# Performance work log

Measured on AMD Instinct MI355X. Metric: run time of the kernel, lower is better.

The kernel has to match this reference:

```python
import jax, jax.numpy as jnp
import numpy as np

B, L, D = 4, 4096, 768
ORDER = 2
EMB = 33      # HyenaFilter emb_dim default
FFN = 64      # filter_order
FREQ = 10.0


def setup_inputs() -> dict:
    key = jax.random.key(0)
    ks = jax.random.split(key, 10)
    def rn(i, shape, scale):
        return jax.random.normal(ks[i], shape, dtype=jnp.float32) * scale
    return {
        "u": jax.random.normal(ks[0], (B, L, D), dtype=jnp.float32),
        "W_in": rn(1, (D, (ORDER + 1) * D), 0.02),
        "b_in": jnp.zeros(((ORDER + 1) * D,), jnp.float32),
        "conv_k": rn(2, (3, (ORDER + 1) * D), 0.3),   # depthwise kernel, 3 taps
        "conv_b": jnp.zeros(((ORDER + 1) * D,), jnp.float32),
        "W1": rn(3, (EMB, FFN), 0.1),
        "b1": jnp.zeros((FFN,), jnp.float32),
        "W2": rn(4, (FFN, ORDER * D), 0.05),
        "b2": jnp.zeros((ORDER * D,), jnp.float32),
        "f_bias": rn(5, (ORDER, D), 0.05),
        "f_decay": rn(6, (ORDER, D), 0.05),
        "W_out": rn(7, (D, D), 0.02),
        "b_out": jnp.zeros((D,), jnp.float32),
    }


def _hyena_filter(W1, b1, W2, b2, f_bias, f_decay):
    # Implicit filter: sinusoidal positional features -> MLP with sin activation
    t = jnp.linspace(0.0, 1.0, L)[:, None]                      # [L,1]
    bands = jnp.linspace(0.0, float(EMB - 1), EMB)[None, :]     # [1,EMB]
    pe = jnp.sin(t * bands * FREQ)                              # [L,EMB]
    h = jnp.sin(FREQ * (pe @ W1 + b1))                          # [L,FFN]
    h = h @ W2 + b2                                             # [L,ORDER*D]
    h = h.reshape(L, ORDER, D).transpose(1, 2, 0)               # [ORDER,D,L]
    t_window = jnp.linspace(0.0, float(L), L)[None, None, :]    # [1,1,L]
    decay = jnp.exp(-jnp.exp(f_decay)[:, :, None] * t_window)   # [ORDER,D,L]
    return h * decay + f_bias[:, :, None]


def reference(u, W_in, b_in, conv_k, conv_b, W1, b1, W2, b2,
              f_bias, f_decay, W_out, b_out):
    # input projection: [B,L,D] -> [B,L,(ORDER+1)*D]
    proj = u @ W_in + b_in
    # depthwise causal conv, kernel_size=3 (pad 2 on the left)
    xp = jnp.pad(proj, ((0, 0), (2, 0), (0, 0)))
    proj = (xp[:, 0:L, :] * conv_k[0]
            + xp[:, 1:L + 1, :] * conv_k[1]
            + xp[:, 2:L + 2, :] * conv_k[2]) + conv_b
    proj = proj.reshape(B, L, ORDER + 1, D).transpose(0, 2, 3, 1)  # [B,ORDER+1,D,L]
    x = proj[:, :ORDER]   # gates, [B,ORDER,D,L]
    v = proj[:, ORDER]    # value, [B,D,L]

    h = _hyena_filter(W1, b1, W2, b2, f_bias, f_decay)  # [ORDER,D,L]

    n_fft = 2 * L  # zero-padded linear convolution via rfft
    for n in range(ORDER):
        v_f = jnp.fft.rfft(v, n=n_fft, axis=-1)          # [B,D,L+1] complex
        h_f = jnp.fft.rfft(h[n], n=n_fft, axis=-1)       # [D,L+1] complex
        y = jnp.fft.irfft(v_f * h_f[None], n=n_fft, axis=-1)[..., :L]
        v = y * x[:, n]                                   # gated recurrence

    return v.transpose(0, 2, 1) @ W_out + b_out           # [B,L,D]
```

## Files before the change

kernel.cpp:

```cpp
#include <hip/hip_runtime.h>
#include <math.h>

#define L_SEQ 4096
#define D_DIM 768
#define C3    2304
#define TAPS  32

typedef __attribute__((ext_vector_type(8))) short bf16x8;
typedef __attribute__((ext_vector_type(4))) float f32x4;

__device__ __forceinline__ unsigned short f2bf(float x) {
  union { float f; unsigned u; } v; v.f = x;
  unsigned r = v.u + 0x7FFF + ((v.u >> 16) & 1);
  return (unsigned short)(r >> 16);
}
__device__ __forceinline__ float bf2f(unsigned short u) {
  union { unsigned u; float f; } v; v.u = ((unsigned)u) << 16; return v.f;
}
__device__ __forceinline__ void gld_lds16(const void* g, void* l) {
  __builtin_amdgcn_global_load_lds((const __attribute__((address_space(1))) void*)g,
                                   (__attribute__((address_space(3))) void*)l, 16, 0, 0);
}

__global__ __launch_bounds__(256) void filt_kernel(const float* __restrict__ W1,
                                                   const float* __restrict__ b1,
                                                   const float* __restrict__ W2,
                                                   const float* __restrict__ b2,
                                                   const float* __restrict__ f_decay,
                                                   float* __restrict__ g_tab) {
  __shared__ float phi_s[2048];
  const int tid = threadIdx.x;
  #pragma unroll
  for (int it = 0; it < 8; ++it) {
    int idx = tid + it * 256;
    int t = idx >> 6, f = idx & 63;
    float tt = (float)t / 4095.0f;
    float s = b1[f];
    #pragma unroll
    for (int e = 0; e < 33; ++e)
      s += sinf(tt * (float)e * 10.0f) * W1[e * 64 + f];
    phi_s[idx] = sinf(10.0f * s);
  }
  __syncthreads();
  int idx = blockIdx.x * 256 + tid;
  int c2 = idx >> 5, t = idx & 31;
  float acc = b2[c2];
  #pragma unroll 8
  for (int f = 0; f < 64; ++f)
    acc += phi_s[t * 64 + f] * W2[f * 1536 + c2];
  float r = expf(f_decay[c2]);
  g_tab[idx] = acc * expf(-r * (float)t * (4096.0f / 4095.0f));
}

__global__ __launch_bounds__(256) void cvt_kernel(const float* __restrict__ src,
                                                  unsigned short* __restrict__ dst) {
  int idx = (blockIdx.x * 256 + threadIdx.x) * 4;
  float4 v = *(const float4*)&src[idx];
  ushort4 o;
  o.x = f2bf(v.x); o.y = f2bf(v.y); o.z = f2bf(v.z); o.w = f2bf(v.w);
  *(ushort4*)&dst[idx] = o;
}

__global__ __launch_bounds__(256) void wtrans_kernel(const float* __restrict__ W_in,
                                                     unsigned short* __restrict__ W_inT,
                                                     const float* __restrict__ W_out,
                                                     unsigned short* __restrict__ W_outT) {
  __shared__ float t[32][33];
  const int z = blockIdx.z;
  const float* src = z ? W_out : W_in;
  unsigned short* dst = z ? W_outT : W_inT;
  const int C = z ? 768 : 2304;
  const int c0 = blockIdx.x * 32, r0 = blockIdx.y * 32;
  if (c0 >= C) return;
  const int tx = threadIdx.x & 31, ty = threadIdx.x >> 5;
  #pragma unroll
  for (int rr = 0; rr < 4; ++rr)
    t[ty + rr * 8][tx] = src[(long)(r0 + ty + rr * 8) * C + c0 + tx];
  __syncthreads();
  #pragma unroll
  for (int rr = 0; rr < 4; ++rr)
    dst[(long)(c0 + ty + rr * 8) * 768 + r0 + tx] = f2bf(t[tx][ty + rr * 8]);
}

__device__ __forceinline__ void g1_vmwait(int VM) {
  if (VM == 8)      asm volatile("s_waitcnt vmcnt(8)" ::: "memory");
  else if (VM == 4) asm volatile("s_waitcnt vmcnt(4)" ::: "memory");
  else if (VM == 0) asm volatile("s_waitcnt vmcnt(0)" ::: "memory");
}

template<bool STG, int VM>
__device__ __forceinline__ void g1_step(int kt, char* smemc, int tid,
                                        int wm128, int wn64, int fm, int csel,
                                        const unsigned short* aP, const unsigned short* bP,
                                        f32x4 (&acc)[8][4]) {
  const int s = kt & 3;
  const unsigned short* As = (const unsigned short*)(smemc + s * 32768);
  const unsigned short* Bs = (const unsigned short*)(smemc + s * 32768 + 16384);
  bf16x8 af[4], bfr[4];
  #pragma unroll
  for (int i = 0; i < 4; ++i) af[i]  = *(const bf16x8*)&As[(wm128 + i * 16 + fm) * 32 + csel];
  #pragma unroll
  for (int jj = 0; jj < 4; ++jj) bfr[jj] = *(const bf16x8*)&Bs[(wn64 + jj * 16 + fm) * 32 + csel];
  if (STG) {
    const unsigned short* ap = aP + (kt + 3) * 32;
    char* d = smemc + ((kt + 3) & 3) * 32768 + tid * 16;
    gld_lds16(ap,         d);
    gld_lds16(ap + 98304, d + 8192);
  }
  asm volatile("" ::: "memory");
  __builtin_amdgcn_s_barrier();
  __builtin_amdgcn_s_setprio(1);
  __builtin_amdgcn_sched_barrier(0);
  #pragma unroll
  for (int i = 0; i < 4; ++i)
    #pragma unroll
    for (int jj = 0; jj < 4; ++jj)
      acc[i][jj] = __builtin_amdgcn_mfma_f32_16x16x32_bf16(af[i], bfr[jj], acc[i][jj], 0, 0, 0);
  __builtin_amdgcn_sched_barrier(0);
  __builtin_amdgcn_s_setprio(0);
  asm volatile("" ::: "memory");
  __builtin_amdgcn_s_barrier();
  bf16x8 ag[4];
  #pragma unroll
  for (int i = 0; i < 4; ++i) ag[i] = *(const bf16x8*)&As[(wm128 + (i + 4) * 16 + fm) * 32 + csel];
  if (STG) {
    const unsigned short* bp = bP + (kt + 3) * 32;
    char* d = smemc + ((kt + 3) & 3) * 32768 + 16384 + tid * 16;
    gld_lds16(bp,         d);
    gld_lds16(bp + 98304, d + 8192);
  }
  asm volatile("" ::: "memory");
  __builtin_amdgcn_s_barrier();
  __builtin_amdgcn_s_setprio(1);
  __builtin_amdgcn_sched_barrier(0);
  #pragma unroll
  for (int i = 0; i < 4; ++i)
    #pragma unroll
    for (int jj = 0; jj < 4; ++jj)
      acc[i + 4][jj] = __builtin_amdgcn_mfma_f32_16x16x32_bf16(ag[i], bfr[jj], acc[i + 4][jj], 0, 0, 0);
  __builtin_amdgcn_sched_barrier(0);
  __builtin_amdgcn_s_setprio(0);
  g1_vmwait(VM);
  asm volatile("" ::: "memory");
  __builtin_amdgcn_s_barrier();
}

__global__ __launch_bounds__(512, 2) void gemm1_8ph(const unsigned short* __restrict__ A,
                                                    const unsigned short* __restrict__ Bt,
                                                    const float* __restrict__ bias,
                                                    unsigned short* __restrict__ proj) {
  extern __shared__ char smemc[];
  const int tid = threadIdx.x;
  const int w = tid >> 6, lane = tid & 63;
  const int id = blockIdx.x;
  const int x8 = id & 7, jb = id >> 3;
  const int mt = x8 * 8 + jb / 9, nt = jb % 9;
  const int m0 = mt * 256, n0 = nt * 256;
  const int wm128 = (w >> 2) * 128, wn64 = (w & 3) * 64;
  const int fm = lane & 15;
  const int csel = (((lane >> 4) ^ ((fm >> 1) & 3)) << 3);
  const int q_src = ((tid & 3) ^ ((tid >> 3) & 3)) * 8;
  const unsigned short* aP = A  + (size_t)(m0 + (tid >> 2)) * 768 + q_src;
  const unsigned short* bP = Bt + (size_t)(n0 + (tid >> 2)) * 768 + q_src;
  f32x4 acc[8][4] = {};

  #pragma unroll
  for (int kt = 0; kt < 3; ++kt) {
    char* d = smemc + kt * 32768 + tid * 16;
    const unsigned short* ap = aP + kt * 32;
    const unsigned short* bp = bP + kt * 32;
    gld_lds16(ap,         d);
    gld_lds16(ap + 98304, d + 8192);
    gld_lds16(bp,         d + 16384);
    gld_lds16(bp + 98304, d + 24576);
  }
  asm volatile("s_waitcnt vmcnt(8)" ::: "memory");
  asm volatile("" ::: "memory");
  __builtin_amdgcn_s_barrier();

  #pragma unroll 1
  for (int kt = 0; kt < 21; ++kt)
    g1_step<true, 8>(kt, smemc, tid, wm128, wn64, fm, csel, aP, bP, acc);
  g1_step<false, 4>(21, smemc, tid, wm128, wn64, fm, csel, aP, bP, acc);
  g1_step<false, 0>(22, smemc, tid, wm128, wn64, fm, csel, aP, bP, acc);
  g1_step<false, -1>(23, smemc, tid, wm128, wn64, fm, csel, aP, bP, acc);

  const int b = m0 >> 12, l0 = m0 & 4095;
  float* fbuf = (float*)smemc + w * 1088;
  const int fk = lane >> 4;
  #pragma unroll
  for (int j2 = 0; j2 < 4; ++j2) {
    #pragma unroll
    for (int ih = 0; ih < 2; ++ih) {
      __syncthreads();
      #pragma unroll
      for (int i = 0; i < 4; ++i)
        *(f32x4*)&fbuf[fm * 68 + i * 16 + fk * 4] = acc[ih * 4 + i][j2];
      __syncthreads();
      #pragma unroll
      for (int p = 0; p < 4; ++p) {
        int nl = p * 4 + fk;
        int c = n0 + wn64 + j2 * 16 + nl;
        float4 v = *(float4*)&fbuf[nl * 68 + fm * 4];
        float bb = bias[c];
        ushort4 o;
        o.x = f2bf(v.x + bb); o.y = f2bf(v.y + bb);
        o.z = f2bf(v.z + bb); o.w = f2bf(v.w + bb);
        *(ushort4*)&proj[((size_t)b * C3 + c) * L_SEQ + l0 + wm128 + ih * 64 + fm * 4] = o;
      }
    }
  }
}

#define G2_BUF 12288
__global__ __launch_bounds__(256) void gemm2_mfma(const unsigned short* __restrict__ A,
                                                  const unsigned short* __restrict__ Bt,
                                                  const float* __restrict__ bias,
                                                  float* __restrict__ out) {
  __shared__ __align__(16) char smem[24576];
  const int tid = threadIdx.x;
  const int w = tid >> 6, lane = tid & 63;
  const int lr = tid >> 2, lc = tid & 3;
  const int id = blockIdx.y * 6 + blockIdx.x;
  const int x8 = id & 7, j = id >> 3;
  const int m0 = (x8 * 32 + j / 6) * 64;
  const int n0 = (j % 6) * 128;
  const int wm = (w & 1) * 32, wn = (w >> 1) * 64;
  const int fm = lane & 15, fk = lane >> 4;
  f32x4 acc[2][4] = {};
  const unsigned short* Ag = A + (size_t)(m0 + lr) * 768 + lc * 8;
  const unsigned short* Bg = Bt + (size_t)(n0 + lr) * 768 + lc * 8;

  {
    char* dst = smem + tid * 16;
    gld_lds16(Ag,            dst);
    gld_lds16(Bg,            dst + 4096);
    gld_lds16(Bg + 64 * 768, dst + 8192);
  }
  for (int kk = 0; kk < 24; ++kk) {
    const int cur = (kk & 1) * G2_BUF;
    __syncthreads();
    if (kk < 23) {
      const int k0 = (kk + 1) * 32;
      char* dst = smem + ((kk + 1) & 1) * G2_BUF + tid * 16;
      gld_lds16(Ag + k0,            dst);
      gld_lds16(Bg + k0,            dst + 4096);
      gld_lds16(Bg + k0 + 64 * 768, dst + 8192);
    }
    const unsigned short* As = (const unsigned short*)(smem + cur);
    const unsigned short* Bs = As + 2048;
    bf16x8 af[2], bfr[4];
    #pragma unroll
    for (int i = 0; i < 2; ++i) af[i]  = *(const bf16x8*)&As[(wm + i * 16 + fm) * 32 + fk * 8];
    #pragma unroll
    for (int j2 = 0; j2 < 4; ++j2) bfr[j2] = *(const bf16x8*)&Bs[(wn + j2 * 16 + fm) * 32 + fk * 8];
    #pragma unroll
    for (int i = 0; i < 2; ++i)
      #pragma unroll
      for (int j2 = 0; j2 < 4; ++j2)
        acc[i][j2] = __builtin_amdgcn_mfma_f32_16x16x32_bf16(af[i], bfr[j2], acc[i][j2], 0, 0, 0);
  }

  float* fbuf = (float*)smem + w * 1088;
  const int nf = lane & 15, mq = lane >> 4;
  float4 bb4 = *(const float4*)&bias[n0 + wn + nf * 4];
  #pragma unroll
  for (int i = 0; i < 2; ++i) {
    __syncthreads();
    #pragma unroll
    for (int cg = 0; cg < 4; ++cg)
      #pragma unroll
      for (int r = 0; r < 4; ++r)
        fbuf[(fk * 4 + r) * 68 + cg * 16 + fm] = acc[i][cg][r];
    __syncthreads();
    #pragma unroll
    for (int pass = 0; pass < 4; ++pass) {
      int m_l = pass * 4 + mq;
      float4 v = *(float4*)&fbuf[m_l * 68 + nf * 4];
      v.x += bb4.x; v.y += bb4.y; v.z += bb4.z; v.w += bb4.w;
      *(float4*)&out[(size_t)(m0 + wm + i * 16 + m_l) * D_DIM + n0 + wn + nf * 4] = v;
    }
  }
}

__global__ __launch_bounds__(256) void row_kernel(const unsigned short* __restrict__ proj,
                                                  unsigned short* __restrict__ v2T,
                                                  const float* __restrict__ conv_k,
                                                  const float* __restrict__ conv_b,
                                                  const float* __restrict__ g_tab,
                                                  const float* __restrict__ f_bias) {
  __shared__ float buf0[4128];
  __shared__ float buf1[4128];
  __shared__ float sgs[2 * TAPS];
  __shared__ float wsum[4];
  __shared__ float bnd[3][4][2];
  const int tid = threadIdx.x;
  const int lane = tid & 63, w = tid >> 6;
  const int b = blockIdx.x / D_DIM, d = blockIdx.x % D_DIM;
  const int g = tid * 16;

  const unsigned short* rowV  = proj + ((size_t)b * C3 + 2 * D_DIM + d) * L_SEQ;
  const unsigned short* rowX0 = proj + ((size_t)b * C3 + d) * L_SEQ;
  const unsigned short* rowX1 = proj + ((size_t)b * C3 + D_DIM + d) * L_SEQ;

  float v[16], x0[16], x1[16];
  #pragma unroll
  for (int k = 0; k < 4; ++k) {
    ushort4 qv = *(const ushort4*)&rowV[g + k * 4];
    v[k * 4] = bf2f(qv.x); v[k * 4 + 1] = bf2f(qv.y); v[k * 4 + 2] = bf2f(qv.z); v[k * 4 + 3] = bf2f(qv.w);
    ushort4 q0 = *(const ushort4*)&rowX0[g + k * 4];
    x0[k * 4] = bf2f(q0.x); x0[k * 4 + 1] = bf2f(q0.y); x0[k * 4 + 2] = bf2f(q0.z); x0[k * 4 + 3] = bf2f(q0.w);
    ushort4 q1 = *(const ushort4*)&rowX1[g + k * 4];
    x1[k * 4] = bf2f(q1.x); x1[k * 4 + 1] = bf2f(q1.y); x1[k * 4 + 2] = bf2f(q1.z); x1[k * 4 + 3] = bf2f(q1.w);
  }

  if (tid < 32) {
    int ph = (tid & 15) * 258 + (tid >> 4);
    buf0[ph] = 0.f; buf1[ph] = 0.f;
  }
  if (tid < 64) sgs[tid] = g_tab[((size_t)((tid >> 5) * D_DIM + d)) * TAPS + (tid & 31)];
  if (lane == 63) {
    bnd[0][w][0] = v[14];  bnd[0][w][1] = v[15];
    bnd[1][w][0] = x0[14]; bnd[1][w][1] = x0[15];
    bnd[2][w][0] = x1[14]; bnd[2][w][1] = x1[15];
  }
  const int cv = 2 * D_DIM + d, cx0 = d, cx1 = D_DIM + d;
  const float kv0 = conv_k[cv],  kv1 = conv_k[C3 + cv],  kv2 = conv_k[2 * C3 + cv],  bv = conv_b[cv];
  const float ka0 = conv_k[cx0], ka1 = conv_k[C3 + cx0], ka2 = conv_k[2 * C3 + cx0], ba = conv_b[cx0];
  const float kb0 = conv_k[cx1], kb1 = conv_k[C3 + cx1], kb2 = conv_k[2 * C3 + cx1], bb = conv_b[cx1];
  const float fb0 = f_bias[d], fb1 = f_bias[D_DIM + d];
  __syncthreads();

  float vm1 = __shfl_up(v[15], 1),  vm2 = __shfl_up(v[14], 1);
  float am1 = __shfl_up(x0[15], 1), am2 = __shfl_up(x0[14], 1);
  float bm1 = __shfl_up(x1[15], 1), bm2 = __shfl_up(x1[14], 1);
  if (lane == 0) {
    if (w > 0) {
      vm2 = bnd[0][w-1][0]; vm1 = bnd[0][w-1][1];
      am2 = bnd[1][w-1][0]; am1 = bnd[1][w-1][1];
      bm2 = bnd[2][w-1][0]; bm1 = bnd[2][w-1][1];
    } else {
      vm1 = vm2 = am1 = am2 = bm1 = bm2 = 0.f;
    }
  }
  float r[16];
  r[0] = vm2 * kv0 + vm1 * kv1 + v[0] * kv2 + bv;
  r[1] = vm1 * kv0 + v[0] * kv1 + v[1] * kv2 + bv;
  #pragma unroll
  for (int i = 2; i < 16; ++i) r[i] = v[i-2] * kv0 + v[i-1] * kv1 + v[i] * kv2 + bv;
  {
    float t0 = am2 * ka0 + am1 * ka1 + x0[0] * ka2 + ba;
    float t1 = am1 * ka0 + x0[0] * ka1 + x0[1] * ka2 + ba;
    #pragma unroll
    for (int i = 15; i >= 2; --i) x0[i] = x0[i-2] * ka0 + x0[i-1] * ka1 + x0[i] * ka2 + ba;
    x0[0] = t0; x0[1] = t1;
  }
  {
    float t0 = bm2 * kb0 + bm1 * kb1 + x1[0] * kb2 + bb;
    float t1 = bm1 * kb0 + x1[0] * kb1 + x1[1] * kb2 + bb;
    #pragma unroll
    for (int i = 15; i >= 2; --i) x1[i] = x1[i-2] * kb0 + x1[i-1] * kb1 + x1[i] * kb2 + bb;
    x1[0] = t0; x1[1] = t1;
  }
  #pragma unroll
  for (int i = 0; i < 16; ++i) buf0[i * 258 + tid + 2] = r[i];
  __syncthreads();

  float h[32];
  #pragma unroll
  for (int j = 0; j < 32; ++j) h[j] = buf0[(j & 15) * 258 + tid + (j >> 4)];
  float p[16], run = 0.f;
  #pragma unroll
  for (int i = 0; i < 16; ++i) { run += r[i]; p[i] = run; }
  float s = run;
  #pragma unroll
  for (int off = 1; off < 64; off <<= 1) {
    float o = __shfl_up(s, off);
    if (lane >= off) s += o;
  }
  if (lane == 63) wsum[w] = s;
  __syncthreads();
  float woff = 0.f;
  #pragma unroll
  for (int k = 0; k < 4; ++k) if (k < w) woff += wsum[k];
  float excl = woff + s - run;
  float y0[16];
  #pragma unroll
  for (int i = 0; i < 16; ++i) {
    float a = fb0 * (excl + p[i]);
    #pragma unroll
    for (int t = 0; t < TAPS; ++t) {
      float vv = (t <= i) ? r[i - t] : h[32 + i - t];
      a += sgs[t] * vv;
    }
    y0[i] = a * x0[i];
  }
  #pragma unroll
  for (int i = 0; i < 16; ++i) buf1[i * 258 + tid + 2] = y0[i];
  __syncthreads();

  #pragma unroll
  for (int j = 0; j < 32; ++j) h[j] = buf1[(j & 15) * 258 + tid + (j >> 4)];
  run = 0.f;
  #pragma unroll
  for (int i = 0; i < 16; ++i) { run += y0[i]; p[i] = run; }
  s = run;
  #pragma unroll
  for (int off = 1; off < 64; off <<= 1) {
    float o = __shfl_up(s, off);
    if (lane >= off) s += o;
  }
  if (lane == 63) wsum[w] = s;
  __syncthreads();
  woff = 0.f;
  #pragma unroll
  for (int k = 0; k < 4; ++k) if (k < w) woff += wsum[k];
  excl = woff + s - run;
  unsigned short yout[16];
  #pragma unroll
  for (int i = 0; i < 16; ++i) {
    float a = fb1 * (excl + p[i]);
    #pragma unroll
    for (int t = 0; t < TAPS; ++t) {
      float vv = (t <= i) ? y0[i - t] : h[32 + i - t];
      a += sgs[TAPS + t] * vv;
    }
    yout[i] = f2bf(a * x1[i]);
  }
  unsigned short* outRow = v2T + ((size_t)b * D_DIM + d) * L_SEQ + g;
  *(ushort4*)&outRow[0]  = *(ushort4*)&yout[0];
  *(ushort4*)&outRow[4]  = *(ushort4*)&yout[4];
  *(ushort4*)&outRow[8]  = *(ushort4*)&yout[8];
  *(ushort4*)&outRow[12] = *(ushort4*)&yout[12];
}

__global__ __launch_bounds__(256) void transpose_v2(const unsigned short* __restrict__ src,
                                                    unsigned short* __restrict__ dst) {
  __shared__ unsigned short t[64][66];
  const int l0 = blockIdx.x * 64, d0 = blockIdx.y * 64, b = blockIdx.z;
  const int tx = threadIdx.x & 31, ty = threadIdx.x >> 5;
  const unsigned short* s = src + ((size_t)b * D_DIM + d0) * L_SEQ + l0;
  #pragma unroll
  for (int r = 0; r < 8; ++r) {
    int dd = ty + r * 8;
    *(ushort2*)&t[dd][tx * 2] = *(const ushort2*)&s[(size_t)dd * L_SEQ + tx * 2];
  }
  __syncthreads();
  unsigned short* q = dst + ((size_t)b * L_SEQ + l0) * D_DIM + d0;
  #pragma unroll
  for (int r = 0; r < 8; ++r) {
    int ll = ty + r * 8;
    ushort2 v; v.x = t[tx * 2][ll]; v.y = t[tx * 2 + 1][ll];
    *(ushort2*)&q[(size_t)ll * D_DIM + tx * 2] = v;
  }
}

extern "C" void kernel_launch(void* const* d_in, const int* in_sizes, int n_in,
                              void* d_out, int out_size, void* d_ws, size_t ws_size,
                              hipStream_t stream) {
  (void)in_sizes; (void)n_in; (void)out_size; (void)ws_size;
  const float* u       = (const float*)d_in[0];
  const float* W_in    = (const float*)d_in[1];
  const float* b_in    = (const float*)d_in[2];
  const float* conv_k  = (const float*)d_in[3];
  const float* conv_b  = (const float*)d_in[4];
  const float* W1      = (const float*)d_in[5];
  const float* b1      = (const float*)d_in[6];
  const float* W2      = (const float*)d_in[7];
  const float* b2      = (const float*)d_in[8];
  const float* f_bias  = (const float*)d_in[9];
  const float* f_decay = (const float*)d_in[10];
  const float* W_out   = (const float*)d_in[11];
  const float* b_out   = (const float*)d_in[12];
  float* out = (float*)d_out;

  unsigned short* proj  = (unsigned short*)d_ws;
  unsigned short* v2T   = proj + (size_t)4 * C3 * L_SEQ;
  unsigned short* ubf   = v2T + (size_t)4 * D_DIM * L_SEQ;
  unsigned short* v2F   = ubf;
  unsigned short* W_inT = ubf + (size_t)16384 * 768;
  unsigned short* W_outT= W_inT + (size_t)C3 * D_DIM;
  float* g_tab          = (float*)(W_outT + (size_t)D_DIM * D_DIM);

  static bool g1_attr = false;
  if (!g1_attr) {
    (void)hipFuncSetAttribute(reinterpret_cast<const void*>(gemm1_8ph),
                              hipFuncAttributeMaxDynamicSharedMemorySize, 131072);
    g1_attr = true;
  }

  filt_kernel<<<192, 256, 0, stream>>>(W1, b1, W2, b2, f_decay, g_tab);
  cvt_kernel<<<12288, 256, 0, stream>>>(u, ubf);
  wtrans_kernel<<<dim3(72, 24, 2), 256, 0, stream>>>(W_in, W_inT, W_out, W_outT);
  gemm1_8ph<<<576, 512, 131072, stream>>>(ubf, W_inT, b_in, proj);
  row_kernel<<<3072, 256, 0, stream>>>(proj, v2T, conv_k, conv_b, g_tab, f_bias);
  transpose_v2<<<dim3(64, 12, 4), 256, 0, stream>>>(v2T, v2F);
  gemm2_mfma<<<dim3(6, 256), 256, 0, stream>>>(v2F, W_outT, b_out, out);
}
```

Before: 310.9 us.

## Shrink gemm1 tile to 256x128 with 3-stage pipeline and higher occupancy

Reworks the input-projection GEMM from 256x256 tiles with a 4-stage, two-phase LDS pipeline to 256x128 tiles with a 3-stage, single-phase pipeline. Each warp now holds a 64x64 accumulator instead of 128x64, LDS use drops from 128KB to 72KB, and the launch bound asks for 4 waves per SIMD, doubling the grid to 1152 blocks. The aim is more occupancy and better latency hiding at the cost of lower per-tile data reuse, more global traffic for A, and more barriers per unit of MFMA work.

```diff
diff --git a/kernel.cpp b/kernel.cpp
--- a/kernel.cpp
+++ b/kernel.cpp
@@ -83,29 +83,29 @@
 }
 
 __device__ __forceinline__ void g1_vmwait(int VM) {
-  if (VM == 8)      asm volatile("s_waitcnt vmcnt(8)" ::: "memory");
-  else if (VM == 4) asm volatile("s_waitcnt vmcnt(4)" ::: "memory");
+  if (VM == 3)      asm volatile("s_waitcnt vmcnt(3)" ::: "memory");
   else if (VM == 0) asm volatile("s_waitcnt vmcnt(0)" ::: "memory");
 }
 
 template<bool STG, int VM>
-__device__ __forceinline__ void g1_step(int kt, char* smemc, int tid,
-                                        int wm128, int wn64, int fm, int csel,
+__device__ __forceinline__ void g1_step(int scur, int sstg, int kt, char* smemc, int tid,
+                                        int wmRow, int wn64, int fm, int csel,
                                         const unsigned short* aP, const unsigned short* bP,
-                                        f32x4 (&acc)[8][4]) {
-  const int s = kt & 3;
-  const unsigned short* As = (const unsigned short*)(smemc + s * 32768);
-  const unsigned short* Bs = (const unsigned short*)(smemc + s * 32768 + 16384);
+                                        f32x4 (&acc)[4][4]) {
+  const unsigned short* As = (const unsigned short*)(smemc + scur * 24576);
+  const unsigned short* Bs = (const unsigned short*)(smemc + scur * 24576 + 16384);
   bf16x8 af[4], bfr[4];
   #pragma unroll
-  for (int i = 0; i < 4; ++i) af[i]  = *(const bf16x8*)&As[(wm128 + i * 16 + fm) * 32 + csel];
+  for (int i = 0; i < 4; ++i) af[i]  = *(const bf16x8*)&As[(wmRow + i * 16 + fm) * 32 + csel];
   #pragma unroll
   for (int jj = 0; jj < 4; ++jj) bfr[jj] = *(const bf16x8*)&Bs[(wn64 + jj * 16 + fm) * 32 + csel];
   if (STG) {
-    const unsigned short* ap = aP + (kt + 3) * 32;
-    char* d = smemc + ((kt + 3) & 3) * 32768 + tid * 16;
+    const unsigned short* ap = aP + (kt + 2) * 32;
+    const unsigned short* bp = bP + (kt + 2) * 32;
+    char* d = smemc + sstg * 24576 + tid * 16;
     gld_lds16(ap,         d);
     gld_lds16(ap + 98304, d + 8192);
+    gld_lds16(bp,         d + 16384);
   }
   asm volatile("" ::: "memory");
   __builtin_amdgcn_s_barrier();
@@ -116,28 +116,6 @@
     #pragma unroll
     for (int jj = 0; jj < 4; ++jj)
       acc[i][jj] = __builtin_amdgcn_mfma_f32_16x16x32_bf16(af[i], bfr[jj], acc[i][jj], 0, 0, 0);
-  __builtin_amdgcn_sched_barrier(0);
-  __builtin_amdgcn_s_setprio(0);
-  asm volatile("" ::: "memory");
-  __builtin_amdgcn_s_barrier();
-  bf16x8 ag[4];
-  #pragma unroll
-  for (int i = 0; i < 4; ++i) ag[i] = *(const bf16x8*)&As[(wm128 + (i + 4) * 16 + fm) * 32 + csel];
-  if (STG) {
-    const unsigned short* bp = bP + (kt + 3) * 32;
-    char* d = smemc + ((kt + 3) & 3) * 32768 + 16384 + tid * 16;
-    gld_lds16(bp,         d);
-    gld_lds16(bp + 98304, d + 8192);
-  }
-  asm volatile("" ::: "memory");
-  __builtin_amdgcn_s_barrier();
-  __builtin_amdgcn_s_setprio(1);
-  __builtin_amdgcn_sched_barrier(0);
-  #pragma unroll
-  for (int i = 0; i < 4; ++i)
-    #pragma unroll
-    for (int jj = 0; jj < 4; ++jj)
-      acc[i + 4][jj] = __builtin_amdgcn_mfma_f32_16x16x32_bf16(ag[i], bfr[jj], acc[i + 4][jj], 0, 0, 0);
   __builtin_amdgcn_sched_barrier(0);
   __builtin_amdgcn_s_setprio(0);
   g1_vmwait(VM);
@@ -145,7 +123,7 @@
   __builtin_amdgcn_s_barrier();
 }
 
-__global__ __launch_bounds__(512, 2) void gemm1_8ph(const unsigned short* __restrict__ A,
+__global__ __launch_bounds__(512, 4) void gemm1_2ph(const unsigned short* __restrict__ A,
                                                     const unsigned short* __restrict__ Bt,
                                                     const float* __restrict__ bias,
                                                     unsigned short* __restrict__ proj) {
@@ -154,60 +132,63 @@
   const int w = tid >> 6, lane = tid & 63;
   const int id = blockIdx.x;
   const int x8 = id & 7, jb = id >> 3;
-  const int mt = x8 * 8 + jb / 9, nt = jb % 9;
-  const int m0 = mt * 256, n0 = nt * 256;
-  const int wm128 = (w >> 2) * 128, wn64 = (w & 3) * 64;
+  const int mt = x8 * 8 + jb / 18, nt = jb % 18;
+  const int m0 = mt * 256, n0 = nt * 128;
+  const int wmRow = (w & 3) * 64, wn64 = (w >> 2) * 64;
   const int fm = lane & 15;
   const int csel = (((lane >> 4) ^ ((fm >> 1) & 3)) << 3);
   const int q_src = ((tid & 3) ^ ((tid >> 3) & 3)) * 8;
   const unsigned short* aP = A  + (size_t)(m0 + (tid >> 2)) * 768 + q_src;
   const unsigned short* bP = Bt + (size_t)(n0 + (tid >> 2)) * 768 + q_src;
-  f32x4 acc[8][4] = {};
-
-  #pragma unroll
-  for (int kt = 0; kt < 3; ++kt) {
-    char* d = smemc + kt * 32768 + tid * 16;
+  f32x4 acc[4][4] = {};
+
+  #pragma unroll
+  for (int kt = 0; kt < 2; ++kt) {
+    char* d = smemc + kt * 24576 + tid * 16;
     const unsigned short* ap = aP + kt * 32;
     const unsigned short* bp = bP + kt * 32;
     gld_lds16(ap,         d);
     gld_lds16(ap + 98304, d + 8192);
     gld_lds16(bp,         d + 16384);
-    gld_lds16(bp + 98304, d + 24576);
-  }
-  asm volatile("s_waitcnt vmcnt(8)" ::: "memory");
+  }
+  asm volatile("s_waitcnt vmcnt(3)" ::: "memory");
   asm volatile("" ::: "memory");
   __builtin_amdgcn_s_barrier();
 
+  int scur = 0;
   #pragma unroll 1
-  for (int kt = 0; kt < 21; ++kt)
-    g1_step<true, 8>(kt, smemc, tid, wm128, wn64, fm, csel, aP, bP, acc);
-  g1_step<false, 4>(21, smemc, tid, wm128, wn64, fm, csel, aP, bP, acc);
-  g1_step<false, 0>(22, smemc, tid, wm128, wn64, fm, csel, aP, bP, acc);
-  g1_step<false, -1>(23, smemc, tid, wm128, wn64, fm, csel, aP, bP, acc);
+  for (int kt = 0; kt < 22; ++kt) {
+    int sstg = scur + 2; if (sstg >= 3) sstg -= 3;
+    g1_step<true, 3>(scur, sstg, kt, smemc, tid, wmRow, wn64, fm, csel, aP, bP, acc);
+    scur = (scur == 2) ? 0 : scur + 1;
+  }
+  {
+    int sstg = scur + 2; if (sstg >= 3) sstg -= 3;
+    g1_step<false, 0>(scur, sstg, 22, smemc, tid, wmRow, wn64, fm, csel, aP, bP, acc);
+    scur = (scur == 2) ? 0 : scur + 1;
+  }
+  g1_step<false, -1>(scur, 0, 23, smemc, tid, wmRow, wn64, fm, csel, aP, bP, acc);
 
   const int b = m0 >> 12, l0 = m0 & 4095;
   float* fbuf = (float*)smemc + w * 1088;
   const int fk = lane >> 4;
   #pragma unroll
   for (int j2 = 0; j2 < 4; ++j2) {
-    #pragma unroll
-    for (int ih = 0; ih < 2; ++ih) {
-      __syncthreads();
-      #pragma unroll
-      for (int i = 0; i < 4; ++i)
-        *(f32x4*)&fbuf[fm * 68 + i * 16 + fk * 4] = acc[ih * 4 + i][j2];
-      __syncthreads();
-      #pragma unroll
-      for (int p = 0; p < 4; ++p) {
-        int nl = p * 4 + fk;
-        int c = n0 + wn64 + j2 * 16 + nl;
-        float4 v = *(float4*)&fbuf[nl * 68 + fm * 4];
-        float bb = bias[c];
-        ushort4 o;
-        o.x = f2bf(v.x + bb); o.y = f2bf(v.y + bb);
-        o.z = f2bf(v.z + bb); o.w = f2bf(v.w + bb);
-        *(ushort4*)&proj[((size_t)b * C3 + c) * L_SEQ + l0 + wm128 + ih * 64 + fm * 4] = o;
-      }
+    __syncthreads();
+    #pragma unroll
+    for (int i = 0; i < 4; ++i)
+      *(f32x4*)&fbuf[fm * 68 + i * 16 + fk * 4] = acc[i][j2];
+    __syncthreads();
+    #pragma unroll
+    for (int p = 0; p < 4; ++p) {
+      int nl = p * 4 + fk;
+      int c = n0 + wn64 + j2 * 16 + nl;
+      float4 v = *(float4*)&fbuf[nl * 68 + fm * 4];
+      float bb = bias[c];
+      ushort4 o;
+      o.x = f2bf(v.x + bb); o.y = f2bf(v.y + bb);
+      o.z = f2bf(v.z + bb); o.w = f2bf(v.w + bb);
+      *(ushort4*)&proj[((size_t)b * C3 + c) * L_SEQ + l0 + wmRow + fm * 4] = o;
     }
   }
 }
@@ -484,15 +465,15 @@
 
   static bool g1_attr = false;
   if (!g1_attr) {
-    (void)hipFuncSetAttribute(reinterpret_cast<const void*>(gemm1_8ph),
-                              hipFuncAttributeMaxDynamicSharedMemorySize, 131072);
+    (void)hipFuncSetAttribute(reinterpret_cast<const void*>(gemm1_2ph),
+                              hipFuncAttributeMaxDynamicSharedMemorySize, 73728);
     g1_attr = true;
   }
 
   filt_kernel<<<192, 256, 0, stream>>>(W1, b1, W2, b2, f_decay, g_tab);
   cvt_kernel<<<12288, 256, 0, stream>>>(u, ubf);
   wtrans_kernel<<<dim3(72, 24, 2), 256, 0, stream>>>(W_in, W_inT, W_out, W_outT);
-  gemm1_8ph<<<576, 512, 131072, stream>>>(ubf, W_inT, b_in, proj);
+  gemm1_2ph<<<1152, 512, 73728, stream>>>(ubf, W_inT, b_in, proj);
   row_kernel<<<3072, 256, 0, stream>>>(proj, v2T, conv_k, conv_b, g_tab, f_bias);
   transpose_v2<<<dim3(64, 12, 4), 256, 0, stream>>>(v2T, v2F);
   gemm2_mfma<<<dim3(6, 256), 256, 0, stream>>>(v2F, W_outT, b_out, out);
```

Measured after the change: 307.7 us. About the same (-1.0%).
